# Performance work log

Measured on AMD Instinct MI355X. Metric: run time of the kernel, lower is better.

Reference implementation:

```python
import jax, jax.numpy as jnp
import numpy as np

B, S, N, H, C = 32, 128, 1024, 2, 128  # batch, seq_len(=in/out channels), num_nodes, heads, out_channels
NEG_SLOPE = 0.2


def setup_inputs() -> dict:
    key = jax.random.key(0)
    k1, k2, k3, k4 = jax.random.split(key, 4)
    scale = 1.0 / np.sqrt(S)
    return {
        "x": jax.random.normal(k1, (B, S, N), dtype=jnp.float32),
        "W": jax.random.normal(k2, (H, S, C), dtype=jnp.float32) * scale,
        "att_src": jax.random.normal(k3, (H, C), dtype=jnp.float32) * scale,
        "att_dst": jax.random.normal(k4, (H, C), dtype=jnp.float32) * scale,
        "bias": jnp.zeros((C,), dtype=jnp.float32),
    }


def reference(x, W, att_src, att_dst, bias):
    # x: [B, S, N] -> node features [B, N, S]
    xt = jnp.transpose(x, (0, 2, 1))
    # per-head projection: z [B, H, N, C]
    z = jnp.einsum('bns,hsc->bhnc', xt, W)
    # scalar attention scores per node: [B, H, N]
    s_src = jnp.einsum('bhnc,hc->bhn', z, att_src)
    s_dst = jnp.einsum('bhnc,hc->bhn', z, att_dst)
    # complete graph: e[i, j] = leaky_relu(s_dst[i] + s_src[j]); softmax over sources j
    e = jax.nn.leaky_relu(s_dst[..., :, None] + s_src[..., None, :], NEG_SLOPE)
    alpha = jax.nn.softmax(e, axis=-1)  # [B, H, N, N]
    out = jnp.einsum('bhij,bhjc->bhic', alpha, z)  # [B, H, N, C]
    out = jnp.mean(out, axis=1) + bias  # concat=False -> mean over heads; [B, N, C]
    return jnp.transpose(out, (0, 2, 1))  # [B, C(=S), N]
```

## Files before the change

### kernel.cpp

```cpp
#include <hip/hip_runtime.h>
#include <hip/hip_bf16.h>
#include <math.h>

constexpr int B_ = 32, S_ = 128, N_ = 1024, H_ = 2, C_ = 128;
#define L2E_ 1.44269504088896340736f

typedef short  bf16x8 __attribute__((ext_vector_type(8)));
typedef float  f32x4  __attribute__((ext_vector_type(4)));
typedef ushort u16x8  __attribute__((ext_vector_type(8)));

__device__ __forceinline__ ushort f2bf(float f) {
    __hip_bfloat16 h = __float2bfloat16(f);
    return __builtin_bit_cast(ushort, h);
}
__device__ __forceinline__ float bfhi(ushort u) {
    return __builtin_bit_cast(float, (uint)u << 16);
}

__global__ __launch_bounds__(512)
void wprep_kernel(const float* __restrict__ W,
                  ushort* __restrict__ wth, ushort* __restrict__ wtl)
{
    __shared__ float sm[128 * 129];
    const int h = blockIdx.x, tid = threadIdx.x;
    const float* Wh = W + (size_t)h * S_ * C_;
#pragma unroll
    for (int it = 0; it < 32; ++it) {
        int e = it * 512 + tid;
        int s = e >> 7, c = e & 127;
        sm[s * 129 + c] = Wh[e];
    }
    __syncthreads();
    const int c = tid >> 2, sg = (tid & 3) * 32;
    const size_t rowb = ((size_t)h * C_ + c) * S_ + sg;
#pragma unroll
    for (int g = 0; g < 4; ++g) {
        u16x8 vh, vl;
#pragma unroll
        for (int e = 0; e < 8; ++e) {
            float v = sm[(sg + g * 8 + e) * 129 + c];
            ushort hh = f2bf(v);
            vh[e] = hh;
            vl[e] = f2bf(v - bfhi(hh));
        }
        *(u16x8*)&wth[rowb + g * 8] = vh;
        *(u16x8*)&wtl[rowb + g * 8] = vl;
    }
}

__global__ __launch_bounds__(512, 2)
void proj_kernel(const float* __restrict__ x,
                 const ushort* __restrict__ wth, const ushort* __restrict__ wtl,
                 const float* __restrict__ att_src, const float* __restrict__ att_dst,
                 ushort* __restrict__ zt, float* __restrict__ ssrc,
                 float* __restrict__ sdst)
{
    const int nb = blockIdx.x * 128;
    const int b  = blockIdx.y;
    const int w = threadIdx.x >> 6, lane = threadIdx.x & 63;
    const int wn = w >> 1, wh = w & 1;
    const int lrow = lane & 15, lq = lane >> 4;
    const size_t bh = (size_t)(b * 2 + wh);

    f32x4 acc[2][8];
#pragma unroll
    for (int tt = 0; tt < 2; ++tt)
#pragma unroll
        for (int ct = 0; ct < 8; ++ct)
#pragma unroll
            for (int r = 0; r < 4; ++r) acc[tt][ct][r] = 0.f;

    const float* xp0 = x + (size_t)b * S_ * N_ + nb + wn * 32 + lrow;
    const size_t wbase = (size_t)wh * C_ * S_ + (size_t)lrow * S_ + lq * 8;

#pragma unroll
    for (int kc = 0; kc < 4; ++kc) {
        bf16x8 ah[2], al[2];
#pragma unroll
        for (int tt = 0; tt < 2; ++tt) {
            const float* xp = xp0 + tt * 16 + (size_t)(kc * 32 + lq * 8) * N_;
#pragma unroll
            for (int e = 0; e < 8; ++e) {
                float v = xp[(size_t)e * N_];
                ushort hi = f2bf(v);
                ah[tt][e] = (short)hi;
                al[tt][e] = (short)f2bf(v - bfhi(hi));
            }
        }
#pragma unroll
        for (int ct = 0; ct < 8; ++ct) {
            const size_t wo = wbase + (size_t)ct * 16 * S_ + kc * 32;
            bf16x8 bhv = *(const bf16x8*)(wth + wo);
            bf16x8 blv = *(const bf16x8*)(wtl + wo);
#pragma unroll
            for (int tt = 0; tt < 2; ++tt) {
                acc[tt][ct] = __builtin_amdgcn_mfma_f32_16x16x32_bf16(ah[tt], bhv, acc[tt][ct], 0, 0, 0);
                acc[tt][ct] = __builtin_amdgcn_mfma_f32_16x16x32_bf16(ah[tt], blv, acc[tt][ct], 0, 0, 0);
                acc[tt][ct] = __builtin_amdgcn_mfma_f32_16x16x32_bf16(al[tt], bhv, acc[tt][ct], 0, 0, 0);
            }
        }
    }

    float asrc[8], adst[8];
#pragma unroll
    for (int ct = 0; ct < 8; ++ct) {
        asrc[ct] = att_src[wh * C_ + ct * 16 + lrow];
        adst[ct] = att_dst[wh * C_ + ct * 16 + lrow];
    }
#pragma unroll
    for (int tt = 0; tt < 2; ++tt)
#pragma unroll
        for (int r = 0; r < 4; ++r) {
            float ps = 0.f, pd = 0.f;
#pragma unroll
            for (int ct = 0; ct < 8; ++ct) {
                ps = fmaf(acc[tt][ct][r], asrc[ct], ps);
                pd = fmaf(acc[tt][ct][r], adst[ct], pd);
            }
#pragma unroll
            for (int msk = 8; msk >= 1; msk >>= 1) {
                ps += __shfl_xor(ps, msk, 64);
                pd += __shfl_xor(pd, msk, 64);
            }
            if (lrow == 0) {
                int n = nb + wn * 32 + tt * 16 + lq * 4 + r;
                ssrc[bh * N_ + n] = ps;
                sdst[bh * N_ + n] = pd;
            }
        }

#pragma unroll
    for (int tt = 0; tt < 2; ++tt)
#pragma unroll
        for (int ct = 0; ct < 8; ++ct) {
            ushort4 v;
            v.x = f2bf(acc[tt][ct][0]); v.y = f2bf(acc[tt][ct][1]);
            v.z = f2bf(acc[tt][ct][2]); v.w = f2bf(acc[tt][ct][3]);
            *(ushort4*)&zt[(bh * C_ + ct * 16 + lrow) * N_ + nb + wn * 32 + tt * 16 + lq * 4] = v;
        }
}

__global__ __launch_bounds__(256)
void lsum_kernel(const float* __restrict__ ssrc, const float* __restrict__ sdst,
                 float* __restrict__ e1t, float* __restrict__ e2t,
                 float* __restrict__ Aar, float* __restrict__ Bar,
                 float* __restrict__ Trar)
{
    const int bh = blockIdx.y, ib = blockIdx.x * 256;
    const int tid = threadIdx.x;
    __shared__ float e1s[N_], e2s[N_];

#pragma unroll
    for (int it = 0; it < 4; ++it) {
        int j = it * 256 + tid;
        float sv = ssrc[(size_t)bh * N_ + j] * L2E_;
        e1s[j] = exp2f(sv);
        e2s[j] = exp2f(0.2f * sv);
    }
    __syncthreads();

    const int i = ib + tid;
    e1t[(size_t)bh * N_ + i] = e1s[i];
    e2t[(size_t)bh * N_ + i] = e2s[i];

    const float dt = sdst[(size_t)bh * N_ + i] * L2E_;
    const float pA = exp2f(dt), pB = exp2f(0.2f * dt), Tr = exp2f(-dt);

    float l0 = 0.f, l1 = 0.f, l2 = 0.f, l3 = 0.f;
    for (int j = 0; j < N_; j += 4) {
        float a0 = e1s[j],     a1 = e1s[j + 1], a2 = e1s[j + 2], a3 = e1s[j + 3];
        float b0 = e2s[j],     b1 = e2s[j + 1], b2 = e2s[j + 2], b3 = e2s[j + 3];
        l0 += (a0 >= Tr) ? pA * a0 : pB * b0;
        l1 += (a1 >= Tr) ? pA * a1 : pB * b1;
        l2 += (a2 >= Tr) ? pA * a2 : pB * b2;
        l3 += (a3 >= Tr) ? pA * a3 : pB * b3;
    }
    const float inv = 0.5f / ((l0 + l1) + (l2 + l3));
    Aar[(size_t)bh * N_ + i]  = pA * inv;
    Bar[(size_t)bh * N_ + i]  = pB * inv;
    Trar[(size_t)bh * N_ + i] = Tr;
}

__device__ __forceinline__ void stage_chunk512(const ushort* __restrict__ zt,
                                               uint* zstage, int b, int w,
                                               int lane, int buf, int j0)
{
#pragma unroll
    for (int it = 0; it < 4; ++it) {
        int id = (w * 4 + it) * 64 + lane;
        int hh = id >> 10, c = (id >> 3) & 127, jq = id & 7;
        const uint* src = (const uint*)(zt + (((size_t)(b * 2 + hh) * C_ + c) * N_)
                                       + j0 + ((jq ^ (c & 7)) << 3));
        __builtin_amdgcn_global_load_lds(
            (const __attribute__((address_space(1))) uint*)src,
            (__attribute__((address_space(3))) uint*)&zstage[buf * 8192 + (w * 4 + it) * 256],
            16, 0, 0);
    }
}

__global__ __launch_bounds__(512, 2)
void attn_kernel(const ushort* __restrict__ zt,
                 const float* __restrict__ e1t, const float* __restrict__ e2t,
                 const float* __restrict__ Aar, const float* __restrict__ Bar,
                 const float* __restrict__ Trar, const float* __restrict__ bias,
                 float* __restrict__ out)
{
    const int id0 = blockIdx.x;
    const int xcd = id0 & 7, k = id0 >> 3;
    const int b = xcd * 4 + (k >> 3), bx = k & 7;

    const int tid = threadIdx.x;
    const int w = tid >> 6, lane = tid & 63;
    const int rg = w >> 2, h = (w >> 1) & 1, js = w & 1;
    const int lrow = lane & 15, lq = lane >> 4;
    const int rowbase = bx * 128 + rg * 64;
    const size_t bh = (size_t)(b * 2 + h);

    __shared__ char pool[128 * 132 * 4];
    __shared__ float e1s[2][N_], e2s[2][N_];
    uint* zstage = (uint*)pool;
    float* exch  = (float*)pool;

    float A4[4], B4[4], T4[4];
#pragma unroll
    for (int t = 0; t < 4; ++t) {
        int i = rowbase + t * 16 + lrow;
        A4[t] = Aar[bh * N_ + i];
        B4[t] = Bar[bh * N_ + i];
        T4[t] = Trar[bh * N_ + i];
    }
#pragma unroll
    for (int it = 0; it < 4; ++it) {
        int e = it * 512 + tid;
        int hh = e >> 10, j = e & 1023;
        e1s[hh][j] = e1t[((size_t)b * 2 + hh) * N_ + j];
        e2s[hh][j] = e2t[((size_t)b * 2 + hh) * N_ + j];
    }
    stage_chunk512(zt, zstage, b, w, lane, 0, 0);
    __syncthreads();

    f32x4 acc[4][8];
#pragma unroll
    for (int t = 0; t < 4; ++t)
#pragma unroll
        for (int ct = 0; ct < 8; ++ct)
#pragma unroll
            for (int r = 0; r < 4; ++r) acc[t][ct][r] = 0.f;

    int buf = 0;
    for (int jc = 0; jc < 16; ++jc) {
        if (jc < 15) stage_chunk512(zt, zstage, b, w, lane, buf ^ 1, (jc + 1) * 64);
        const int j32 = jc * 64 + js * 32;

        float4 e1a = *(const float4*)&e1s[h][j32 + lq * 8];
        float4 e1b = *(const float4*)&e1s[h][j32 + lq * 8 + 4];
        float4 e2a = *(const float4*)&e2s[h][j32 + lq * 8];
        float4 e2b = *(const float4*)&e2s[h][j32 + lq * 8 + 4];
        float ev1[8] = {e1a.x, e1a.y, e1a.z, e1a.w, e1b.x, e1b.y, e1b.z, e1b.w};
        float ev2[8] = {e2a.x, e2a.y, e2a.z, e2a.w, e2b.x, e2b.y, e2b.z, e2b.w};

        bf16x8 bf[8];
#pragma unroll
        for (int ct = 0; ct < 8; ++ct) {
            int c = ct * 16 + lrow;
            int off = buf * 32768 + h * 16384 + c * 128 + ((((js * 4) + lq) ^ (c & 7)) << 4);
            bf[ct] = *(const bf16x8*)((const char*)zstage + off);
        }
#pragma unroll
        for (int t = 0; t < 4; ++t) {
            bf16x8 af;
#pragma unroll
            for (int r = 0; r < 8; ++r) {
                float al = (ev1[r] >= T4[t]) ? A4[t] * ev1[r] : B4[t] * ev2[r];
                af[r] = (short)f2bf(al);
            }
#pragma unroll
            for (int ct = 0; ct < 8; ++ct)
                acc[t][ct] = __builtin_amdgcn_mfma_f32_16x16x32_bf16(af, bf[ct], acc[t][ct], 0, 0, 0);
        }
        __syncthreads();
        buf ^= 1;
    }

    const int grp = w & 3;
#pragma unroll 1
    for (int p = 0; p < 4; ++p) {
        if (grp == p) {
#pragma unroll
            for (int t = 0; t < 4; ++t)
#pragma unroll
                for (int ct = 0; ct < 8; ++ct) {
                    int c = ct * 16 + lrow;
                    int i = rg * 64 + t * 16 + lq * 4;
                    float* dst = &exch[c * 132 + i];
                    if (p == 0) {
                        *(float4*)dst = make_float4(acc[t][ct][0], acc[t][ct][1],
                                                    acc[t][ct][2], acc[t][ct][3]);
                    } else {
                        float4 v = *(const float4*)dst;
                        v.x += acc[t][ct][0]; v.y += acc[t][ct][1];
                        v.z += acc[t][ct][2]; v.w += acc[t][ct][3];
                        *(float4*)dst = v;
                    }
                }
        }
        __syncthreads();
    }

    const int cl = tid >> 5, il = (tid & 31) * 4;
#pragma unroll
    for (int it = 0; it < 8; ++it) {
        int c = it * 16 + cl;
        float bvv = bias[c];
        float4 v = *(const float4*)&exch[c * 132 + il];
        v.x += bvv; v.y += bvv; v.z += bvv; v.w += bvv;
        *(float4*)&out[((size_t)b * C_ + c) * N_ + bx * 128 + il] = v;
    }
}

extern "C" void kernel_launch(void* const* d_in, const int* in_sizes, int n_in,
                              void* d_out, int out_size, void* d_ws, size_t ws_size,
                              hipStream_t stream) {
    const float* x       = (const float*)d_in[0];
    const float* W       = (const float*)d_in[1];
    const float* att_src = (const float*)d_in[2];
    const float* att_dst = (const float*)d_in[3];
    const float* bias    = (const float*)d_in[4];
    float* out = (float*)d_out;

    ushort* wth = (ushort*)d_ws;
    ushort* wtl = wth + (size_t)H_ * C_ * S_;
    ushort* zt  = wtl + (size_t)H_ * C_ * S_;
    float* ssrc = (float*)(zt + (size_t)B_ * H_ * C_ * N_);
    float* sdst = ssrc + (size_t)B_ * H_ * N_;
    float* e1t  = sdst + (size_t)B_ * H_ * N_;
    float* e2t  = e1t + (size_t)B_ * H_ * N_;
    float* Aar  = e2t + (size_t)B_ * H_ * N_;
    float* Bar  = Aar + (size_t)B_ * H_ * N_;
    float* Trar = Bar + (size_t)B_ * H_ * N_;

    wprep_kernel<<<dim3(2), 512, 0, stream>>>(W, wth, wtl);
    proj_kernel<<<dim3(8, 32), 512, 0, stream>>>(
        x, wth, wtl, att_src, att_dst, zt, ssrc, sdst);
    lsum_kernel<<<dim3(4, B_ * H_), 256, 0, stream>>>(
        ssrc, sdst, e1t, e2t, Aar, Bar, Trar);
    attn_kernel<<<dim3(256), 512, 0, stream>>>(
        zt, e1t, e2t, Aar, Bar, Trar, bias, out);
}
```

Before: 171.9 us.

## Fuse softmax normalizer into attention kernel and rework projection and weight prep

Drops the separate lsum kernel. The attention kernel now computes the exponentials and per-row softmax sums itself in shared memory, which removes one launch and the global round trips for the e1/e2/A/B/Tr arrays. Each projection wave now handles both heads for 16 nodes, so it loads and splits x once per head pair. Weight prep uses more blocks, and the library bf16 conversion is replaced by bit-manipulation truncate and round helpers. The attention LDS address math is hoisted out of the loop. The cost is redundant exponential and sum work in each attention block, plus different rounding behaviour.

```diff
diff --git a/kernel.cpp b/kernel.cpp
--- a/kernel.cpp
+++ b/kernel.cpp
@@ -9,39 +9,43 @@
 typedef float  f32x4  __attribute__((ext_vector_type(4)));
 typedef ushort u16x8  __attribute__((ext_vector_type(8)));
 
-__device__ __forceinline__ ushort f2bf(float f) {
-    __hip_bfloat16 h = __float2bfloat16(f);
-    return __builtin_bit_cast(ushort, h);
+__device__ __forceinline__ ushort bfr(float f) {
+    uint u = __builtin_bit_cast(uint, f);
+    return (ushort)((u + 0x8000u) >> 16);
+}
+__device__ __forceinline__ ushort bft(float f) {
+    return (ushort)(__builtin_bit_cast(uint, f) >> 16);
 }
 __device__ __forceinline__ float bfhi(ushort u) {
     return __builtin_bit_cast(float, (uint)u << 16);
 }
 
-__global__ __launch_bounds__(512)
+__global__ __launch_bounds__(256)
 void wprep_kernel(const float* __restrict__ W,
                   ushort* __restrict__ wth, ushort* __restrict__ wtl)
 {
-    __shared__ float sm[128 * 129];
-    const int h = blockIdx.x, tid = threadIdx.x;
-    const float* Wh = W + (size_t)h * S_ * C_;
-#pragma unroll
-    for (int it = 0; it < 32; ++it) {
-        int e = it * 512 + tid;
-        int s = e >> 7, c = e & 127;
-        sm[s * 129 + c] = Wh[e];
+    __shared__ float sm[128][33];
+    const int h = blockIdx.x >> 2, cb = (blockIdx.x & 3) * 32;
+    const int tid = threadIdx.x;
+    const float* Wh = W + (size_t)h * S_ * C_ + cb;
+#pragma unroll
+    for (int it = 0; it < 16; ++it) {
+        int e = it * 256 + tid;
+        int s = e >> 5, c = e & 31;
+        sm[s][c] = Wh[s * C_ + c];
     }
     __syncthreads();
-    const int c = tid >> 2, sg = (tid & 3) * 32;
-    const size_t rowb = ((size_t)h * C_ + c) * S_ + sg;
-#pragma unroll
-    for (int g = 0; g < 4; ++g) {
+    const int c = tid >> 3, sg = (tid & 7) * 16;
+    const size_t rowb = ((size_t)h * C_ + cb + c) * S_ + sg;
+#pragma unroll
+    for (int g = 0; g < 2; ++g) {
         u16x8 vh, vl;
 #pragma unroll
         for (int e = 0; e < 8; ++e) {
-            float v = sm[(sg + g * 8 + e) * 129 + c];
-            ushort hh = f2bf(v);
+            float v = sm[sg + g * 8 + e][c];
+            ushort hh = bft(v);
             vh[e] = hh;
-            vl[e] = f2bf(v - bfhi(hh));
+            vl[e] = bfr(v - bfhi(hh));
         }
         *(u16x8*)&wth[rowb + g * 8] = vh;
         *(u16x8*)&wtl[rowb + g * 8] = vl;
@@ -58,64 +62,59 @@
     const int nb = blockIdx.x * 128;
     const int b  = blockIdx.y;
     const int w = threadIdx.x >> 6, lane = threadIdx.x & 63;
-    const int wn = w >> 1, wh = w & 1;
     const int lrow = lane & 15, lq = lane >> 4;
-    const size_t bh = (size_t)(b * 2 + wh);
 
     f32x4 acc[2][8];
 #pragma unroll
-    for (int tt = 0; tt < 2; ++tt)
+    for (int h = 0; h < 2; ++h)
 #pragma unroll
         for (int ct = 0; ct < 8; ++ct)
 #pragma unroll
-            for (int r = 0; r < 4; ++r) acc[tt][ct][r] = 0.f;
-
-    const float* xp0 = x + (size_t)b * S_ * N_ + nb + wn * 32 + lrow;
-    const size_t wbase = (size_t)wh * C_ * S_ + (size_t)lrow * S_ + lq * 8;
+            for (int r = 0; r < 4; ++r) acc[h][ct][r] = 0.f;
+
+    const float* xp0 = x + (size_t)b * S_ * N_ + nb + w * 16 + lrow;
 
 #pragma unroll
     for (int kc = 0; kc < 4; ++kc) {
-        bf16x8 ah[2], al[2];
-#pragma unroll
-        for (int tt = 0; tt < 2; ++tt) {
-            const float* xp = xp0 + tt * 16 + (size_t)(kc * 32 + lq * 8) * N_;
-#pragma unroll
-            for (int e = 0; e < 8; ++e) {
-                float v = xp[(size_t)e * N_];
-                ushort hi = f2bf(v);
-                ah[tt][e] = (short)hi;
-                al[tt][e] = (short)f2bf(v - bfhi(hi));
-            }
-        }
+        bf16x8 ah, al;
+        const float* xp = xp0 + (size_t)(kc * 32 + lq * 8) * N_;
+#pragma unroll
+        for (int e = 0; e < 8; ++e) {
+            float v = xp[(size_t)e * N_];
+            ushort hi = bft(v);
+            ah[e] = (short)hi;
+            al[e] = (short)bfr(v - bfhi(hi));
+        }
+#pragma unroll
+        for (int h = 0; h < 2; ++h) {
+            const size_t wb = ((size_t)h * C_ + lrow) * S_ + kc * 32 + lq * 8;
+#pragma unroll
+            for (int ct = 0; ct < 8; ++ct) {
+                bf16x8 bhv = *(const bf16x8*)(wth + wb + (size_t)ct * 16 * S_);
+                bf16x8 blv = *(const bf16x8*)(wtl + wb + (size_t)ct * 16 * S_);
+                acc[h][ct] = __builtin_amdgcn_mfma_f32_16x16x32_bf16(ah, bhv, acc[h][ct], 0, 0, 0);
+                acc[h][ct] = __builtin_amdgcn_mfma_f32_16x16x32_bf16(ah, blv, acc[h][ct], 0, 0, 0);
+                acc[h][ct] = __builtin_amdgcn_mfma_f32_16x16x32_bf16(al, bhv, acc[h][ct], 0, 0, 0);
+            }
+        }
+    }
+
+#pragma unroll
+    for (int h = 0; h < 2; ++h) {
+        const size_t bh = (size_t)(b * 2 + h);
+        float asrc[8], adst[8];
 #pragma unroll
         for (int ct = 0; ct < 8; ++ct) {
-            const size_t wo = wbase + (size_t)ct * 16 * S_ + kc * 32;
-            bf16x8 bhv = *(const bf16x8*)(wth + wo);
-            bf16x8 blv = *(const bf16x8*)(wtl + wo);
-#pragma unroll
-            for (int tt = 0; tt < 2; ++tt) {
-                acc[tt][ct] = __builtin_amdgcn_mfma_f32_16x16x32_bf16(ah[tt], bhv, acc[tt][ct], 0, 0, 0);
-                acc[tt][ct] = __builtin_amdgcn_mfma_f32_16x16x32_bf16(ah[tt], blv, acc[tt][ct], 0, 0, 0);
-                acc[tt][ct] = __builtin_amdgcn_mfma_f32_16x16x32_bf16(al[tt], bhv, acc[tt][ct], 0, 0, 0);
-            }
-        }
-    }
-
-    float asrc[8], adst[8];
-#pragma unroll
-    for (int ct = 0; ct < 8; ++ct) {
-        asrc[ct] = att_src[wh * C_ + ct * 16 + lrow];
-        adst[ct] = att_dst[wh * C_ + ct * 16 + lrow];
-    }
-#pragma unroll
-    for (int tt = 0; tt < 2; ++tt)
+            asrc[ct] = att_src[h * C_ + ct * 16 + lrow];
+            adst[ct] = att_dst[h * C_ + ct * 16 + lrow];
+        }
 #pragma unroll
         for (int r = 0; r < 4; ++r) {
             float ps = 0.f, pd = 0.f;
 #pragma unroll
             for (int ct = 0; ct < 8; ++ct) {
-                ps = fmaf(acc[tt][ct][r], asrc[ct], ps);
-                pd = fmaf(acc[tt][ct][r], adst[ct], pd);
+                ps = fmaf(acc[h][ct][r], asrc[ct], ps);
+                pd = fmaf(acc[h][ct][r], adst[ct], pd);
             }
 #pragma unroll
             for (int msk = 8; msk >= 1; msk >>= 1) {
@@ -123,62 +122,19 @@
                 pd += __shfl_xor(pd, msk, 64);
             }
             if (lrow == 0) {
-                int n = nb + wn * 32 + tt * 16 + lq * 4 + r;
+                int n = nb + w * 16 + lq * 4 + r;
                 ssrc[bh * N_ + n] = ps;
                 sdst[bh * N_ + n] = pd;
             }
         }
-
-#pragma unroll
-    for (int tt = 0; tt < 2; ++tt)
 #pragma unroll
         for (int ct = 0; ct < 8; ++ct) {
             ushort4 v;
-            v.x = f2bf(acc[tt][ct][0]); v.y = f2bf(acc[tt][ct][1]);
-            v.z = f2bf(acc[tt][ct][2]); v.w = f2bf(acc[tt][ct][3]);
-            *(ushort4*)&zt[(bh * C_ + ct * 16 + lrow) * N_ + nb + wn * 32 + tt * 16 + lq * 4] = v;
-        }
-}
-
-__global__ __launch_bounds__(256)
-void lsum_kernel(const float* __restrict__ ssrc, const float* __restrict__ sdst,
-                 float* __restrict__ e1t, float* __restrict__ e2t,
-                 float* __restrict__ Aar, float* __restrict__ Bar,
-                 float* __restrict__ Trar)
-{
-    const int bh = blockIdx.y, ib = blockIdx.x * 256;
-    const int tid = threadIdx.x;
-    __shared__ float e1s[N_], e2s[N_];
-
-#pragma unroll
-    for (int it = 0; it < 4; ++it) {
-        int j = it * 256 + tid;
-        float sv = ssrc[(size_t)bh * N_ + j] * L2E_;
-        e1s[j] = exp2f(sv);
-        e2s[j] = exp2f(0.2f * sv);
-    }
-    __syncthreads();
-
-    const int i = ib + tid;
-    e1t[(size_t)bh * N_ + i] = e1s[i];
-    e2t[(size_t)bh * N_ + i] = e2s[i];
-
-    const float dt = sdst[(size_t)bh * N_ + i] * L2E_;
-    const float pA = exp2f(dt), pB = exp2f(0.2f * dt), Tr = exp2f(-dt);
-
-    float l0 = 0.f, l1 = 0.f, l2 = 0.f, l3 = 0.f;
-    for (int j = 0; j < N_; j += 4) {
-        float a0 = e1s[j],     a1 = e1s[j + 1], a2 = e1s[j + 2], a3 = e1s[j + 3];
-        float b0 = e2s[j],     b1 = e2s[j + 1], b2 = e2s[j + 2], b3 = e2s[j + 3];
-        l0 += (a0 >= Tr) ? pA * a0 : pB * b0;
-        l1 += (a1 >= Tr) ? pA * a1 : pB * b1;
-        l2 += (a2 >= Tr) ? pA * a2 : pB * b2;
-        l3 += (a3 >= Tr) ? pA * a3 : pB * b3;
-    }
-    const float inv = 0.5f / ((l0 + l1) + (l2 + l3));
-    Aar[(size_t)bh * N_ + i]  = pA * inv;
-    Bar[(size_t)bh * N_ + i]  = pB * inv;
-    Trar[(size_t)bh * N_ + i] = Tr;
+            v.x = bfr(acc[h][ct][0]); v.y = bfr(acc[h][ct][1]);
+            v.z = bfr(acc[h][ct][2]); v.w = bfr(acc[h][ct][3]);
+            *(ushort4*)&zt[(bh * C_ + ct * 16 + lrow) * N_ + nb + w * 16 + lq * 4] = v;
+        }
+    }
 }
 
 __device__ __forceinline__ void stage_chunk512(const ushort* __restrict__ zt,
@@ -199,10 +155,8 @@
 }
 
 __global__ __launch_bounds__(512, 2)
-void attn_kernel(const ushort* __restrict__ zt,
-                 const float* __restrict__ e1t, const float* __restrict__ e2t,
-                 const float* __restrict__ Aar, const float* __restrict__ Bar,
-                 const float* __restrict__ Trar, const float* __restrict__ bias,
+void attn_kernel(const ushort* __restrict__ zt, const float* __restrict__ ssrc,
+                 const float* __restrict__ sdst, const float* __restrict__ bias,
                  float* __restrict__ out)
 {
     const int id0 = blockIdx.x;
@@ -218,26 +172,55 @@
 
     __shared__ char pool[128 * 132 * 4];
     __shared__ float e1s[2][N_], e2s[2][N_];
+    __shared__ float Lpart[512];
+    __shared__ float rowA[2][128], rowB[2][128], rowTr[2][128];
     uint* zstage = (uint*)pool;
     float* exch  = (float*)pool;
 
-    float A4[4], B4[4], T4[4];
-#pragma unroll
-    for (int t = 0; t < 4; ++t) {
-        int i = rowbase + t * 16 + lrow;
-        A4[t] = Aar[bh * N_ + i];
-        B4[t] = Bar[bh * N_ + i];
-        T4[t] = Trar[bh * N_ + i];
-    }
 #pragma unroll
     for (int it = 0; it < 4; ++it) {
         int e = it * 512 + tid;
         int hh = e >> 10, j = e & 1023;
-        e1s[hh][j] = e1t[((size_t)b * 2 + hh) * N_ + j];
-        e2s[hh][j] = e2t[((size_t)b * 2 + hh) * N_ + j];
-    }
+        float sv = ssrc[((size_t)b * 2 + hh) * N_ + j] * L2E_;
+        e1s[hh][j] = exp2f(sv);
+        e2s[hh][j] = exp2f(0.2f * sv);
+    }
+    __syncthreads();
+
     stage_chunk512(zt, zstage, b, w, lane, 0, 0);
+
+    const int rid = tid & 255;
+    const int hh2 = rid >> 7, iloc = rid & 127;
+    const int jh = tid >> 8;
+    const float dt = sdst[((size_t)b * 2 + hh2) * N_ + bx * 128 + iloc] * L2E_;
+    const float pA = exp2f(dt), pB = exp2f(0.2f * dt), Tr = exp2f(-dt);
+    {
+        float L = 0.f;
+        const int j0 = jh * 512;
+        for (int j = j0; j < j0 + 512; j += 4) {
+#pragma unroll
+            for (int u = 0; u < 4; ++u) {
+                float a = e1s[hh2][j + u], bb = e2s[hh2][j + u];
+                L += (a >= Tr) ? pA * a : pB * bb;
+            }
+        }
+        Lpart[tid] = L;
+    }
     __syncthreads();
+    if (tid < 256) {
+        float inv = 0.5f / (Lpart[tid] + Lpart[tid + 256]);
+        rowA[hh2][iloc] = pA * inv;
+        rowB[hh2][iloc] = pB * inv;
+        rowTr[hh2][iloc] = Tr;
+    }
+    __syncthreads();
+
+    float A4[4], B4[4], T4[4];
+#pragma unroll
+    for (int t = 0; t < 4; ++t) {
+        int i = rg * 64 + t * 16 + lrow;
+        A4[t] = rowA[h][i]; B4[t] = rowB[h][i]; T4[t] = rowTr[h][i];
+    }
 
     f32x4 acc[4][8];
 #pragma unroll
@@ -246,6 +229,8 @@
         for (int ct = 0; ct < 8; ++ct)
 #pragma unroll
             for (int r = 0; r < 4; ++r) acc[t][ct][r] = 0.f;
+
+    const int lds_base = h * 16384 + lrow * 128 + (((js * 4 + lq) ^ (lrow & 7)) << 4);
 
     int buf = 0;
     for (int jc = 0; jc < 16; ++jc) {
@@ -259,20 +244,19 @@
         float ev1[8] = {e1a.x, e1a.y, e1a.z, e1a.w, e1b.x, e1b.y, e1b.z, e1b.w};
         float ev2[8] = {e2a.x, e2a.y, e2a.z, e2a.w, e2b.x, e2b.y, e2b.z, e2b.w};
 
+        const char* zb = (const char*)zstage + buf * 32768 + lds_base;
         bf16x8 bf[8];
 #pragma unroll
-        for (int ct = 0; ct < 8; ++ct) {
-            int c = ct * 16 + lrow;
-            int off = buf * 32768 + h * 16384 + c * 128 + ((((js * 4) + lq) ^ (c & 7)) << 4);
-            bf[ct] = *(const bf16x8*)((const char*)zstage + off);
-        }
+        for (int ct = 0; ct < 8; ++ct)
+            bf[ct] = *(const bf16x8*)(zb + ct * 2048);
+
 #pragma unroll
         for (int t = 0; t < 4; ++t) {
             bf16x8 af;
 #pragma unroll
             for (int r = 0; r < 8; ++r) {
                 float al = (ev1[r] >= T4[t]) ? A4[t] * ev1[r] : B4[t] * ev2[r];
-                af[r] = (short)f2bf(al);
+                af[r] = (short)bfr(al);
             }
 #pragma unroll
             for (int ct = 0; ct < 8; ++ct)
@@ -333,17 +317,9 @@
     ushort* zt  = wtl + (size_t)H_ * C_ * S_;
     float* ssrc = (float*)(zt + (size_t)B_ * H_ * C_ * N_);
     float* sdst = ssrc + (size_t)B_ * H_ * N_;
-    float* e1t  = sdst + (size_t)B_ * H_ * N_;
-    float* e2t  = e1t + (size_t)B_ * H_ * N_;
-    float* Aar  = e2t + (size_t)B_ * H_ * N_;
-    float* Bar  = Aar + (size_t)B_ * H_ * N_;
-    float* Trar = Bar + (size_t)B_ * H_ * N_;
-
-    wprep_kernel<<<dim3(2), 512, 0, stream>>>(W, wth, wtl);
+
+    wprep_kernel<<<dim3(8), 256, 0, stream>>>(W, wth, wtl);
     proj_kernel<<<dim3(8, 32), 512, 0, stream>>>(
         x, wth, wtl, att_src, att_dst, zt, ssrc, sdst);
-    lsum_kernel<<<dim3(4, B_ * H_), 256, 0, stream>>>(
-        ssrc, sdst, e1t, e2t, Aar, Bar, Trar);
-    attn_kernel<<<dim3(256), 512, 0, stream>>>(
-        zt, e1t, e2t, Aar, Bar, Trar, bias, out);
-}
+    attn_kernel<<<dim3(256), 512, 0, stream>>>(zt, ssrc, sdst, bias, out);
+}
```

Measured after the change: 280.3 us. 63.0% more time.
